# Kernel optimization log

Measured on AMD Instinct MI355X. Metric: run time of the kernel, lower is better.

The kernel has to match this reference:

```python
import jax, jax.numpy as jnp
import numpy as np

NUM_HEADS = 16
HIDDEN = 1024
MASKED_BIAS = -10000.0


def setup_inputs() -> dict:
    key = jax.random.key(0)
    k1, k2 = jax.random.split(key)
    encodings = jax.random.normal(k1, (4, 2048, HIDDEN), dtype=jnp.float32)
    W_attn = jax.random.normal(k2, (HIDDEN, 3 * HIDDEN), dtype=jnp.float32) * (HIDDEN ** -0.5)
    b_attn = jnp.zeros((3 * HIDDEN,), dtype=jnp.float32)
    return {"encodings": encodings, "W_attn": W_attn, "b_attn": b_attn}


def reference(encodings, W_attn, b_attn):
    b, s, hidden = encodings.shape
    head_size = hidden // NUM_HEADS
    cattn = encodings @ W_attn + b_attn  # [b, s, 3*hidden]
    q, k, v = jnp.split(cattn, 3, axis=-1)
    # [b, s, hidden] -> [b, h, s, c]
    def split_heads(x):
        return x.reshape(b, s, NUM_HEADS, head_size).transpose(0, 2, 1, 3)
    q, k, v = split_heads(q), split_heads(k), split_heads(v)
    scores = jnp.einsum('bhfc,bhtc->bhft', q, k) / np.sqrt(head_size).astype(np.float32)
    causal = jnp.tril(jnp.ones((s, s), dtype=bool))[None, None]
    scores = jnp.where(causal, scores, jnp.float32(MASKED_BIAS))
    patterns = jax.nn.softmax(scores, axis=-1)
    ctx = jnp.einsum('bhft,bhtc->bhfc', patterns, v)
    # [b, h, s, c] -> [b, s, hidden]
    return ctx.transpose(0, 2, 1, 3).reshape(b, s, hidden)
```

## Files before the change

### kernel.cpp

```cpp
#include <hip/hip_runtime.h>

#define B_   4
#define S_   2048
#define HID  1024
#define NH   16
#define CH   64
#define M_   (B_ * S_)
#define N3   (3 * HID)
#define LDT2 72

typedef __attribute__((ext_vector_type(4))) float f32x4;
typedef __attribute__((ext_vector_type(8))) unsigned short u16x8;
typedef __attribute__((ext_vector_type(4))) unsigned short u16x4;

__device__ __forceinline__ unsigned short f2bf(float x) {
    unsigned u = __builtin_bit_cast(unsigned, x);
    u += 0x7fffu + ((u >> 16) & 1u);
    return (unsigned short)(u >> 16);
}
__device__ __forceinline__ float bf2f(unsigned short h) {
    unsigned u = ((unsigned)h) << 16;
    return __builtin_bit_cast(float, u);
}
__device__ __forceinline__ f32x4 mfma16(u16x8 a, u16x8 b, f32x4 c) {
    asm("v_mfma_f32_16x16x32_bf16 %0, %1, %2, %0" : "+v"(c) : "v"(a), "v"(b));
    return c;
}

__global__ __launch_bounds__(256) void k_split(const float* __restrict__ x,
                                               unsigned short* __restrict__ hi,
                                               unsigned short* __restrict__ lo,
                                               int n8) {
    int idx = blockIdx.x * 256 + threadIdx.x;
    if (idx >= n8) return;
    const f32x4* px = (const f32x4*)x + (size_t)idx * 2;
    f32x4 a = px[0], b = px[1];
    u16x8 h, l;
#pragma unroll
    for (int i = 0; i < 8; i++) {
        float xv = (i < 4) ? a[i] : b[i - 4];
        unsigned short hb = f2bf(xv);
        h[i] = hb;
        l[i] = f2bf(xv - bf2f(hb));
    }
    *(u16x8*)(hi + (size_t)idx * 8) = h;
    *(u16x8*)(lo + (size_t)idx * 8) = l;
}

__global__ __launch_bounds__(256) void k_tsplit(const float* __restrict__ W,
                                                unsigned short* __restrict__ WTh,
                                                unsigned short* __restrict__ WTl) {
    __shared__ float tile[32][33];
    int n0 = blockIdx.x * 32, k0 = blockIdx.y * 32;
    int tid = threadIdx.x;
    int r = tid >> 3, c0 = (tid & 7) * 4;
    f32x4 v = *(const f32x4*)(W + (size_t)(k0 + r) * N3 + n0 + c0);
#pragma unroll
    for (int i = 0; i < 4; i++) tile[r][c0 + i] = v[i];
    __syncthreads();
    u16x4 h, l;
#pragma unroll
    for (int i = 0; i < 4; i++) {
        float xv = tile[c0 + i][r];
        unsigned short hb = f2bf(xv);
        h[i] = hb;
        l[i] = f2bf(xv - bf2f(hb));
    }
    size_t o = (size_t)(n0 + r) * HID + k0 + c0;
    *(u16x4*)(WTh + o) = h;
    *(u16x4*)(WTl + o) = l;
}

__global__ __launch_bounds__(256, 2) void k_gemm(
    const unsigned short* __restrict__ Ah, const unsigned short* __restrict__ Al,
    const unsigned short* __restrict__ Bh, const unsigned short* __restrict__ Bl,
    const float* __restrict__ bias,
    unsigned short* __restrict__ Qh, unsigned short* __restrict__ Ql,
    unsigned short* __restrict__ Kh, unsigned short* __restrict__ Kl,
    unsigned short* __restrict__ Vt) {
    __shared__ __attribute__((aligned(16))) unsigned short sAh[128 * LDT2];
    __shared__ __attribute__((aligned(16))) unsigned short sAl[128 * LDT2];
    __shared__ __attribute__((aligned(16))) unsigned short sBh[128 * LDT2];
    __shared__ __attribute__((aligned(16))) unsigned short sBl[128 * LDT2];
    int tid = threadIdx.x;
    int m0 = blockIdx.y * 128, n0 = blockIdx.x * 128;
    int r = tid >> 1, kh2 = (tid & 1) * 32;
    int lane = tid & 63, w = tid >> 6;
    int wm = (w >> 1) * 64, wn = (w & 1) * 64;
    int l15 = lane & 15, l4 = lane >> 4;
    f32x4 acc[4][4] = {};
    size_t gA = (size_t)(m0 + r) * HID + kh2;
    size_t gB = (size_t)(n0 + r) * HID + kh2;

    u16x8 pf[4][4];
#pragma unroll
    for (int j = 0; j < 4; j++) {
        pf[0][j] = *(const u16x8*)(Ah + gA + j * 8);
        pf[1][j] = *(const u16x8*)(Al + gA + j * 8);
        pf[2][j] = *(const u16x8*)(Bh + gB + j * 8);
        pf[3][j] = *(const u16x8*)(Bl + gB + j * 8);
    }
#pragma unroll
    for (int j = 0; j < 4; j++) {
        *(u16x8*)&sAh[r * LDT2 + kh2 + j * 8] = pf[0][j];
        *(u16x8*)&sAl[r * LDT2 + kh2 + j * 8] = pf[1][j];
        *(u16x8*)&sBh[r * LDT2 + kh2 + j * 8] = pf[2][j];
        *(u16x8*)&sBl[r * LDT2 + kh2 + j * 8] = pf[3][j];
    }

    for (int k0 = 0; k0 < HID; k0 += 64) {
        __syncthreads();
        bool more = (k0 + 64 < HID);
        if (more) {
#pragma unroll
            for (int j = 0; j < 4; j++) {
                pf[0][j] = *(const u16x8*)(Ah + gA + k0 + 64 + j * 8);
                pf[1][j] = *(const u16x8*)(Al + gA + k0 + 64 + j * 8);
                pf[2][j] = *(const u16x8*)(Bh + gB + k0 + 64 + j * 8);
                pf[3][j] = *(const u16x8*)(Bl + gB + k0 + 64 + j * 8);
            }
        }
#pragma unroll
        for (int ks = 0; ks < 64; ks += 32) {
            u16x8 a0[4], a1[4], b0[4], b1[4];
#pragma unroll
            for (int i = 0; i < 4; i++) {
                int off = ks + l4 * 8;
                int row = wm + i * 16 + l15;
                a0[i] = *(const u16x8*)&sAh[row * LDT2 + off];
                a1[i] = *(const u16x8*)&sAl[row * LDT2 + off];
                int rowb = wn + i * 16 + l15;
                b0[i] = *(const u16x8*)&sBh[rowb * LDT2 + off];
                b1[i] = *(const u16x8*)&sBl[rowb * LDT2 + off];
            }
#pragma unroll
            for (int mt = 0; mt < 4; mt++)
#pragma unroll
                for (int nt = 0; nt < 4; nt++) {
                    acc[mt][nt] = mfma16(a0[mt], b0[nt], acc[mt][nt]);
                    acc[mt][nt] = mfma16(a0[mt], b1[nt], acc[mt][nt]);
                    acc[mt][nt] = mfma16(a1[mt], b0[nt], acc[mt][nt]);
                }
        }
        __syncthreads();
        if (more) {
#pragma unroll
            for (int j = 0; j < 4; j++) {
                *(u16x8*)&sAh[r * LDT2 + kh2 + j * 8] = pf[0][j];
                *(u16x8*)&sAl[r * LDT2 + kh2 + j * 8] = pf[1][j];
                *(u16x8*)&sBh[r * LDT2 + kh2 + j * 8] = pf[2][j];
                *(u16x8*)&sBl[r * LDT2 + kh2 + j * 8] = pf[3][j];
            }
        }
    }

#pragma unroll
    for (int mt = 0; mt < 4; mt++)
#pragma unroll
        for (int nt = 0; nt < 4; nt++) {
            int n = n0 + wn + nt * 16 + l15;
            float bv = bias[n];
            int which = n >> 10, hid = n & 1023;
            int h = hid >> 6, c = hid & 63;
            int mbase = m0 + wm + mt * 16 + l4 * 4;
            int b = mbase >> 11, sbase = mbase & 2047;
            int bh = b * NH + h;
            if (which == 2) {
                u16x4 pv;
#pragma unroll
                for (int jj = 0; jj < 4; jj++) pv[jj] = f2bf(acc[mt][nt][jj] + bv);
                *(u16x4*)(Vt + ((size_t)bh * CH + c) * S_ + sbase) = pv;
            } else {
                unsigned short* __restrict__ dh = (which == 0) ? Qh : Kh;
                unsigned short* __restrict__ dl = (which == 0) ? Ql : Kl;
                float sc = (which == 0) ? 0.125f : 1.0f;
#pragma unroll
                for (int jj = 0; jj < 4; jj++) {
                    float val = (acc[mt][nt][jj] + bv) * sc;
                    unsigned short hb = f2bf(val);
                    size_t so = ((size_t)bh * S_ + sbase + jj) * CH + c;
                    dh[so] = hb;
                    dl[so] = f2bf(val - bf2f(hb));
                }
            }
        }
}

__global__ __launch_bounds__(256, 2) void k_attn(const unsigned short* __restrict__ Qh,
                                                 const unsigned short* __restrict__ Ql,
                                                 const unsigned short* __restrict__ Kh,
                                                 const unsigned short* __restrict__ Kl,
                                                 const unsigned short* __restrict__ Vt,
                                                 float* __restrict__ out) {
    __shared__ __attribute__((aligned(16))) unsigned short sKbuf[2 * 128 * 64];
    __shared__ __attribute__((aligned(16))) unsigned short sVT[64 * 128];
    char* const sKhB = (char*)sKbuf;
    char* const sKlB = (char*)sKbuf + 16384;
    int tid = threadIdx.x, lane = tid & 63, w = tid >> 6;
    int l15 = lane & 15, l4 = lane >> 4;
    char* const sPB = (char*)sKbuf + w * 8192;
    int qt = gridDim.x - 1 - blockIdx.x;
    int bh = blockIdx.y;
    int b = bh >> 4, h = bh & 15;
    size_t head_off = (size_t)bh * S_ * CH;
    const unsigned short* Qhp = Qh + head_off;
    const unsigned short* Qlp = Ql + head_off;
    const unsigned short* Khp = Kh + head_off;
    const unsigned short* Klp = Kl + head_off;
    const unsigned short* Vtp = Vt + (size_t)bh * CH * S_;

    u16x8 qh[2][2], ql[2][2];
#pragma unroll
    for (int m = 0; m < 2; m++)
#pragma unroll
        for (int cc = 0; cc < 2; cc++) {
            size_t o = (size_t)(qt * 128 + w * 32 + m * 16 + l15) * CH + cc * 32 + l4 * 8;
            qh[m][cc] = *(const u16x8*)(Qhp + o);
            ql[m][cc] = *(const u16x8*)(Qlp + o);
        }

    f32x4 ctx[2][4] = {};
    float mrun[2][4], lrun[2][4];
#pragma unroll
    for (int m = 0; m < 2; m++)
#pragma unroll
        for (int j = 0; j < 4; j++) { mrun[m][j] = -1e30f; lrun[m][j] = 0.f; }

    for (int kt = 0; kt <= qt; kt++) {
        __syncthreads();
#pragma unroll
        for (int j = 0; j < 4; j++) {
            int idx = tid + j * 256;
            int rr = idx >> 3, slot = idx & 7;
            size_t g = (size_t)(kt * 128 + rr) * CH + slot * 8;
            int bo = (slot * 16) ^ ((rr & 7) << 4);
            *(u16x8*)(sKhB + rr * 128 + bo) = *(const u16x8*)(Khp + g);
            *(u16x8*)(sKlB + rr * 128 + bo) = *(const u16x8*)(Klp + g);
        }
#pragma unroll
        for (int j = 0; j < 4; j++) {
            int idx = tid + j * 256;
            int cc = idx >> 4, slot = idx & 15;
            size_t g = (size_t)cc * S_ + kt * 128 + slot * 8;
            int bo = (slot * 16) ^ ((cc & 15) << 4);
            *(u16x8*)((char*)sVT + cc * 256 + bo) = *(const u16x8*)(Vtp + g);
        }
        __syncthreads();

        f32x4 sa[2][8];
#pragma unroll
        for (int m = 0; m < 2; m++)
#pragma unroll
            for (int nt = 0; nt < 8; nt++) sa[m][nt] = f32x4{0.f, 0.f, 0.f, 0.f};
        __builtin_amdgcn_s_setprio(1);
#pragma unroll
        for (int nt = 0; nt < 8; nt++) {
            int rowb = nt * 16 + l15;
            int swb = (rowb & 7) << 4;
            u16x8 kbh[2], kbl[2];
#pragma unroll
            for (int cc = 0; cc < 2; cc++) {
                int off = (cc * 64 + l4 * 16) ^ swb;
                kbh[cc] = *(const u16x8*)(sKhB + rowb * 128 + off);
                kbl[cc] = *(const u16x8*)(sKlB + rowb * 128 + off);
            }
#pragma unroll
            for (int m = 0; m < 2; m++)
#pragma unroll
                for (int cc = 0; cc < 2; cc++) {
                    sa[m][nt] = mfma16(qh[m][cc], kbh[cc], sa[m][nt]);
                    sa[m][nt] = mfma16(qh[m][cc], kbl[cc], sa[m][nt]);
                    sa[m][nt] = mfma16(ql[m][cc], kbh[cc], sa[m][nt]);
                }
        }
        __builtin_amdgcn_s_setprio(0);
        if (kt == qt) {
#pragma unroll
            for (int m = 0; m < 2; m++)
#pragma unroll
                for (int nt = 0; nt < 8; nt++) {
                    int t = nt * 16 + l15;
#pragma unroll
                    for (int jj = 0; jj < 4; jj++) {
                        int f = w * 32 + m * 16 + l4 * 4 + jj;
                        if (t > f) sa[m][nt][jj] = -10000.0f;
                    }
                }
        }
        __syncthreads();

#pragma unroll
        for (int m = 0; m < 2; m++)
#pragma unroll
            for (int jj = 0; jj < 4; jj++) {
                float rx = sa[m][0][jj];
#pragma unroll
                for (int nt = 1; nt < 8; nt++) rx = fmaxf(rx, sa[m][nt][jj]);
                rx = fmaxf(rx, __shfl_xor(rx, 1));
                rx = fmaxf(rx, __shfl_xor(rx, 2));
                rx = fmaxf(rx, __shfl_xor(rx, 4));
                rx = fmaxf(rx, __shfl_xor(rx, 8));
                float mnew = fmaxf(mrun[m][jj], rx);
                float sc = __expf(mrun[m][jj] - mnew);
                mrun[m][jj] = mnew;
                float ps = 0.f;
                int fm = m * 16 + l4 * 4 + jj;
                int swp = (fm & 15) << 4;
#pragma unroll
                for (int nt = 0; nt < 8; nt++) {
                    float p = __expf(sa[m][nt][jj] - mnew);
                    ps += p;
                    int bo = ((nt * 16 + l15) * 2) ^ swp;
                    *(unsigned short*)(sPB + fm * 256 + bo) = f2bf(p);
                }
                lrun[m][jj] = lrun[m][jj] * sc + ps;
#pragma unroll
                for (int nc = 0; nc < 4; nc++) ctx[m][nc][jj] *= sc;
            }
        __builtin_amdgcn_s_setprio(1);
#pragma unroll
        for (int tk = 0; tk < 4; tk++) {
            u16x8 pa[2];
#pragma unroll
            for (int m = 0; m < 2; m++) {
                int row = m * 16 + l15;
                int off = (tk * 64 + l4 * 16) ^ ((row & 15) << 4);
                pa[m] = *(const u16x8*)(sPB + row * 256 + off);
            }
#pragma unroll
            for (int nc = 0; nc < 4; nc++) {
                int rowv = nc * 16 + l15;
                int off = (tk * 64 + l4 * 16) ^ ((rowv & 15) << 4);
                u16x8 vb = *(const u16x8*)((char*)sVT + rowv * 256 + off);
#pragma unroll
                for (int m = 0; m < 2; m++) ctx[m][nc] = mfma16(pa[m], vb, ctx[m][nc]);
            }
        }
        __builtin_amdgcn_s_setprio(0);
    }
#pragma unroll
    for (int m = 0; m < 2; m++)
#pragma unroll
        for (int jj = 0; jj < 4; jj++) {
            float ls = lrun[m][jj];
            ls += __shfl_xor(ls, 1);
            ls += __shfl_xor(ls, 2);
            ls += __shfl_xor(ls, 4);
            ls += __shfl_xor(ls, 8);
            float inv = 1.0f / ls;
            int f = qt * 128 + w * 32 + m * 16 + l4 * 4 + jj;
#pragma unroll
            for (int nc = 0; nc < 4; nc++) {
                int c = nc * 16 + l15;
                out[((size_t)(b * S_ + f)) * HID + h * CH + c] = ctx[m][nc][jj] * inv;
            }
        }
}

extern "C" void kernel_launch(void* const* d_in, const int* in_sizes, int n_in,
                              void* d_out, int out_size, void* d_ws, size_t ws_size,
                              hipStream_t stream) {
    const float* enc  = (const float*)d_in[0];
    const float* W    = (const float*)d_in[1];
    const float* bias = (const float*)d_in[2];
    float* out = (float*)d_out;

    unsigned short* A_hi = (unsigned short*)d_ws;
    unsigned short* A_lo = A_hi + (size_t)M_ * HID;
    unsigned short* WTh  = A_lo + (size_t)M_ * HID;
    unsigned short* WTl  = WTh + (size_t)N3 * HID;
    unsigned short* Qh   = WTl + (size_t)N3 * HID;
    unsigned short* Ql   = Qh + (size_t)M_ * HID;
    unsigned short* Kh   = Ql + (size_t)M_ * HID;
    unsigned short* Kl   = Kh + (size_t)M_ * HID;
    unsigned short* Vt   = Kl + (size_t)M_ * HID;

    int n8 = (M_ * HID) / 8;
    k_split<<<dim3(n8 / 256), 256, 0, stream>>>(enc, A_hi, A_lo, n8);
    k_tsplit<<<dim3(N3 / 32, HID / 32), 256, 0, stream>>>(W, WTh, WTl);
    k_gemm<<<dim3(N3 / 128, M_ / 128), 256, 0, stream>>>(A_hi, A_lo, WTh, WTl, bias,
                                                         Qh, Ql, Kh, Kl, Vt);
    k_attn<<<dim3(S_ / 128, B_ * NH), 256, 0, stream>>>(Qh, Ql, Kh, Kl, Vt, out);
}
```

Baseline: 537.4 us.

## Prefetch next K/V tile into registers during softmax and PV compute

Result: slower. 719.5 us (+33.9%).

```diff
diff --git a/kernel.cpp b/kernel.cpp
--- a/kernel.cpp
+++ b/kernel.cpp
@@ -209,6 +209,19 @@
     const unsigned short* Klp = Kl + head_off;
     const unsigned short* Vtp = Vt + (size_t)bh * CH * S_;
 
+    int kld[4], vld[4];
+    size_t kg[4], vg[4];
+#pragma unroll
+    for (int j = 0; j < 4; j++) {
+        int idx = tid + j * 256;
+        int rr = idx >> 3, sl = idx & 7;
+        kld[j] = rr * 128 + ((sl * 16) ^ ((rr & 7) << 4));
+        kg[j]  = (size_t)rr * CH + sl * 8;
+        int cc = idx >> 4, sv = idx & 15;
+        vld[j] = cc * 256 + ((sv * 16) ^ ((cc & 15) << 4));
+        vg[j]  = (size_t)cc * S_ + sv * 8;
+    }
+
     u16x8 qh[2][2], ql[2][2];
 #pragma unroll
     for (int m = 0; m < 2; m++)
@@ -226,25 +239,17 @@
 #pragma unroll
         for (int j = 0; j < 4; j++) { mrun[m][j] = -1e30f; lrun[m][j] = 0.f; }
 
+#pragma unroll
+    for (int j = 0; j < 4; j++) {
+        u16x8 a = *(const u16x8*)(Khp + kg[j]);
+        u16x8 c = *(const u16x8*)(Klp + kg[j]);
+        u16x8 v = *(const u16x8*)(Vtp + vg[j]);
+        *(u16x8*)(sKhB + kld[j]) = a;
+        *(u16x8*)(sKlB + kld[j]) = c;
+        *(u16x8*)((char*)sVT + vld[j]) = v;
+    }
+
     for (int kt = 0; kt <= qt; kt++) {
-        __syncthreads();
-#pragma unroll
-        for (int j = 0; j < 4; j++) {
-            int idx = tid + j * 256;
-            int rr = idx >> 3, slot = idx & 7;
-            size_t g = (size_t)(kt * 128 + rr) * CH + slot * 8;
-            int bo = (slot * 16) ^ ((rr & 7) << 4);
-            *(u16x8*)(sKhB + rr * 128 + bo) = *(const u16x8*)(Khp + g);
-            *(u16x8*)(sKlB + rr * 128 + bo) = *(const u16x8*)(Klp + g);
-        }
-#pragma unroll
-        for (int j = 0; j < 4; j++) {
-            int idx = tid + j * 256;
-            int cc = idx >> 4, slot = idx & 15;
-            size_t g = (size_t)cc * S_ + kt * 128 + slot * 8;
-            int bo = (slot * 16) ^ ((cc & 15) << 4);
-            *(u16x8*)((char*)sVT + cc * 256 + bo) = *(const u16x8*)(Vtp + g);
-        }
         __syncthreads();
 
         f32x4 sa[2][8];
@@ -288,6 +293,19 @@
                 }
         }
         __syncthreads();
+
+        bool more = (kt < qt);
+        u16x8 pfh[4], pfl[4], pfv[4];
+        if (more) {
+            size_t ko = (size_t)(kt + 1) * 128 * CH;
+            size_t vo = (size_t)(kt + 1) * 128;
+#pragma unroll
+            for (int j = 0; j < 4; j++) {
+                pfh[j] = *(const u16x8*)(Khp + ko + kg[j]);
+                pfl[j] = *(const u16x8*)(Klp + ko + kg[j]);
+                pfv[j] = *(const u16x8*)(Vtp + vo + vg[j]);
+            }
+        }
 
 #pragma unroll
         for (int m = 0; m < 2; m++)
@@ -337,6 +355,16 @@
             }
         }
         __builtin_amdgcn_s_setprio(0);
+
+        __syncthreads();
+        if (more) {
+#pragma unroll
+            for (int j = 0; j < 4; j++) {
+                *(u16x8*)(sKhB + kld[j]) = pfh[j];
+                *(u16x8*)(sKlB + kld[j]) = pfl[j];
+                *(u16x8*)((char*)sVT + vld[j]) = pfv[j];
+            }
+        }
     }
 #pragma unroll
     for (int m = 0; m < 2; m++)
```

## Compute transposed score tiles so each lane owns one query row

Applied to the files above, without the earlier changes.

Result: faster. 478.0 us (-11.1%).

```diff
diff --git a/kernel.cpp b/kernel.cpp
--- a/kernel.cpp
+++ b/kernel.cpp
@@ -211,20 +211,16 @@
 
     u16x8 qh[2][2], ql[2][2];
 #pragma unroll
-    for (int m = 0; m < 2; m++)
+    for (int nf = 0; nf < 2; nf++)
 #pragma unroll
         for (int cc = 0; cc < 2; cc++) {
-            size_t o = (size_t)(qt * 128 + w * 32 + m * 16 + l15) * CH + cc * 32 + l4 * 8;
-            qh[m][cc] = *(const u16x8*)(Qhp + o);
-            ql[m][cc] = *(const u16x8*)(Qlp + o);
-        }
-
-    f32x4 ctx[2][4] = {};
-    float mrun[2][4], lrun[2][4];
-#pragma unroll
-    for (int m = 0; m < 2; m++)
-#pragma unroll
-        for (int j = 0; j < 4; j++) { mrun[m][j] = -1e30f; lrun[m][j] = 0.f; }
+            size_t o = (size_t)(qt * 128 + w * 32 + nf * 16 + l15) * CH + cc * 32 + l4 * 8;
+            qh[nf][cc] = *(const u16x8*)(Qhp + o);
+            ql[nf][cc] = *(const u16x8*)(Qlp + o);
+        }
+
+    f32x4 ctx[4][2] = {};
+    float mrun[2] = {-1e30f, -1e30f}, lrun[2] = {0.f, 0.f};
 
     for (int kt = 0; kt <= qt; kt++) {
         __syncthreads();
@@ -247,114 +243,114 @@
         }
         __syncthreads();
 
-        f32x4 sa[2][8];
-#pragma unroll
-        for (int m = 0; m < 2; m++)
-#pragma unroll
-            for (int nt = 0; nt < 8; nt++) sa[m][nt] = f32x4{0.f, 0.f, 0.f, 0.f};
+        f32x4 sa[8][2];
+#pragma unroll
+        for (int mt = 0; mt < 8; mt++)
+#pragma unroll
+            for (int nf = 0; nf < 2; nf++) sa[mt][nf] = f32x4{0.f, 0.f, 0.f, 0.f};
         __builtin_amdgcn_s_setprio(1);
 #pragma unroll
-        for (int nt = 0; nt < 8; nt++) {
-            int rowb = nt * 16 + l15;
-            int swb = (rowb & 7) << 4;
+        for (int mt = 0; mt < 8; mt++) {
+            int row = mt * 16 + l15;
+            int sw = (row & 7) << 4;
             u16x8 kbh[2], kbl[2];
 #pragma unroll
             for (int cc = 0; cc < 2; cc++) {
-                int off = (cc * 64 + l4 * 16) ^ swb;
-                kbh[cc] = *(const u16x8*)(sKhB + rowb * 128 + off);
-                kbl[cc] = *(const u16x8*)(sKlB + rowb * 128 + off);
-            }
-#pragma unroll
-            for (int m = 0; m < 2; m++)
+                int off = (cc * 64 + l4 * 16) ^ sw;
+                kbh[cc] = *(const u16x8*)(sKhB + row * 128 + off);
+                kbl[cc] = *(const u16x8*)(sKlB + row * 128 + off);
+            }
+#pragma unroll
+            for (int nf = 0; nf < 2; nf++)
 #pragma unroll
                 for (int cc = 0; cc < 2; cc++) {
-                    sa[m][nt] = mfma16(qh[m][cc], kbh[cc], sa[m][nt]);
-                    sa[m][nt] = mfma16(qh[m][cc], kbl[cc], sa[m][nt]);
-                    sa[m][nt] = mfma16(ql[m][cc], kbh[cc], sa[m][nt]);
+                    sa[mt][nf] = mfma16(kbh[cc], qh[nf][cc], sa[mt][nf]);
+                    sa[mt][nf] = mfma16(kbl[cc], qh[nf][cc], sa[mt][nf]);
+                    sa[mt][nf] = mfma16(kbh[cc], ql[nf][cc], sa[mt][nf]);
                 }
         }
         __builtin_amdgcn_s_setprio(0);
         if (kt == qt) {
 #pragma unroll
-            for (int m = 0; m < 2; m++)
-#pragma unroll
-                for (int nt = 0; nt < 8; nt++) {
-                    int t = nt * 16 + l15;
+            for (int mt = 0; mt < 8; mt++)
+#pragma unroll
+                for (int nf = 0; nf < 2; nf++) {
+                    int fq = w * 32 + nf * 16 + l15;
 #pragma unroll
                     for (int jj = 0; jj < 4; jj++) {
-                        int f = w * 32 + m * 16 + l4 * 4 + jj;
-                        if (t > f) sa[m][nt][jj] = -10000.0f;
+                        int t = mt * 16 + l4 * 4 + jj;
+                        if (t > fq) sa[mt][nf][jj] = -10000.0f;
                     }
                 }
         }
         __syncthreads();
 
 #pragma unroll
-        for (int m = 0; m < 2; m++)
-#pragma unroll
-            for (int jj = 0; jj < 4; jj++) {
-                float rx = sa[m][0][jj];
-#pragma unroll
-                for (int nt = 1; nt < 8; nt++) rx = fmaxf(rx, sa[m][nt][jj]);
-                rx = fmaxf(rx, __shfl_xor(rx, 1));
-                rx = fmaxf(rx, __shfl_xor(rx, 2));
-                rx = fmaxf(rx, __shfl_xor(rx, 4));
-                rx = fmaxf(rx, __shfl_xor(rx, 8));
-                float mnew = fmaxf(mrun[m][jj], rx);
-                float sc = __expf(mrun[m][jj] - mnew);
-                mrun[m][jj] = mnew;
-                float ps = 0.f;
-                int fm = m * 16 + l4 * 4 + jj;
-                int swp = (fm & 15) << 4;
-#pragma unroll
-                for (int nt = 0; nt < 8; nt++) {
-                    float p = __expf(sa[m][nt][jj] - mnew);
+        for (int nf = 0; nf < 2; nf++) {
+            float pm = sa[0][nf][0];
+#pragma unroll
+            for (int mt = 0; mt < 8; mt++)
+#pragma unroll
+                for (int jj = 0; jj < 4; jj++) pm = fmaxf(pm, sa[mt][nf][jj]);
+            pm = fmaxf(pm, __shfl_xor(pm, 16));
+            pm = fmaxf(pm, __shfl_xor(pm, 32));
+            float mnew = fmaxf(mrun[nf], pm);
+            float sc = __expf(mrun[nf] - mnew);
+            mrun[nf] = mnew;
+            int fl = nf * 16 + l15;
+            int swp = (fl & 15) << 4;
+            float ps = 0.f;
+#pragma unroll
+            for (int mt = 0; mt < 8; mt++) {
+                u16x4 pv4;
+#pragma unroll
+                for (int jj = 0; jj < 4; jj++) {
+                    float p = __expf(sa[mt][nf][jj] - mnew);
                     ps += p;
-                    int bo = ((nt * 16 + l15) * 2) ^ swp;
-                    *(unsigned short*)(sPB + fm * 256 + bo) = f2bf(p);
-                }
-                lrun[m][jj] = lrun[m][jj] * sc + ps;
-#pragma unroll
-                for (int nc = 0; nc < 4; nc++) ctx[m][nc][jj] *= sc;
-            }
+                    pv4[jj] = f2bf(p);
+                }
+                *(u16x4*)(sPB + fl * 256 + ((mt * 32 + l4 * 8) ^ swp)) = pv4;
+            }
+            ps += __shfl_xor(ps, 16);
+            ps += __shfl_xor(ps, 32);
+            lrun[nf] = lrun[nf] * sc + ps;
+#pragma unroll
+            for (int mc = 0; mc < 4; mc++) ctx[mc][nf] *= sc;
+        }
+
         __builtin_amdgcn_s_setprio(1);
 #pragma unroll
         for (int tk = 0; tk < 4; tk++) {
-            u16x8 pa[2];
-#pragma unroll
-            for (int m = 0; m < 2; m++) {
-                int row = m * 16 + l15;
-                int off = (tk * 64 + l4 * 16) ^ ((row & 15) << 4);
-                pa[m] = *(const u16x8*)(sPB + row * 256 + off);
-            }
-#pragma unroll
-            for (int nc = 0; nc < 4; nc++) {
-                int rowv = nc * 16 + l15;
+            u16x8 pb[2];
+#pragma unroll
+            for (int nf = 0; nf < 2; nf++) {
+                int fl = nf * 16 + l15;
+                int off = (tk * 64 + l4 * 16) ^ ((fl & 15) << 4);
+                pb[nf] = *(const u16x8*)(sPB + fl * 256 + off);
+            }
+#pragma unroll
+            for (int mc = 0; mc < 4; mc++) {
+                int rowv = mc * 16 + l15;
                 int off = (tk * 64 + l4 * 16) ^ ((rowv & 15) << 4);
                 u16x8 vb = *(const u16x8*)((char*)sVT + rowv * 256 + off);
 #pragma unroll
-                for (int m = 0; m < 2; m++) ctx[m][nc] = mfma16(pa[m], vb, ctx[m][nc]);
+                for (int nf = 0; nf < 2; nf++) ctx[mc][nf] = mfma16(vb, pb[nf], ctx[mc][nf]);
             }
         }
         __builtin_amdgcn_s_setprio(0);
     }
 #pragma unroll
-    for (int m = 0; m < 2; m++)
-#pragma unroll
-        for (int jj = 0; jj < 4; jj++) {
-            float ls = lrun[m][jj];
-            ls += __shfl_xor(ls, 1);
-            ls += __shfl_xor(ls, 2);
-            ls += __shfl_xor(ls, 4);
-            ls += __shfl_xor(ls, 8);
-            float inv = 1.0f / ls;
-            int f = qt * 128 + w * 32 + m * 16 + l4 * 4 + jj;
-#pragma unroll
-            for (int nc = 0; nc < 4; nc++) {
-                int c = nc * 16 + l15;
-                out[((size_t)(b * S_ + f)) * HID + h * CH + c] = ctx[m][nc][jj] * inv;
-            }
-        }
+    for (int nf = 0; nf < 2; nf++) {
+        float inv = 1.0f / lrun[nf];
+        int fg = qt * 128 + w * 32 + nf * 16 + l15;
+        float* op = out + ((size_t)(b * S_ + fg)) * HID + h * CH + l4 * 4;
+#pragma unroll
+        for (int mc = 0; mc < 4; mc++) {
+            f32x4 o = ctx[mc][nf];
+            o[0] *= inv; o[1] *= inv; o[2] *= inv; o[3] *= inv;
+            *(f32x4*)(op + mc * 16) = o;
+        }
+    }
 }
 
 extern "C" void kernel_launch(void* const* d_in, const int* in_sizes, int n_in,
```
